# Optimization experiments

Hardware: AMD Instinct MI355X
Metric: run time of the kernel (lower is better)

## Reference

```python
import jax, jax.numpy as jnp
import numpy as np

RADIUS = 0.2
NSAMPLE = 32


def setup_inputs() -> dict:
    key = jax.random.key(0)
    k1, k2 = jax.random.split(key)
    B, N = 8, 4096
    xyz = jax.random.uniform(k1, (B, N, 3), dtype=jnp.float32)
    xyz_new = jax.random.uniform(k2, (B, N, 3), dtype=jnp.float32)  # ignored by forward, kept for signature fidelity
    return {"xyz": xyz, "xyz_new": xyz_new}


def _ball_query(radius, nsample, xyz, new_xyz):
    # xyz: [B, N, 3] source points; new_xyz: [B, M, 3] query centers.
    # Returns idx: [B, M, nsample] int32, matching pointnet2 CUDA ball_query:
    # first `nsample` indices j (in increasing j order) with ||q - p_j||^2 < r^2;
    # unused slots are filled with the first valid index.
    B, N, _ = xyz.shape
    sq_src = jnp.sum(xyz * xyz, axis=-1)          # [B, N]
    sq_q = jnp.sum(new_xyz * new_xyz, axis=-1)    # [B, M]
    # d2[b, m, n] = ||q_m - p_n||^2
    d2 = sq_q[:, :, None] + sq_src[:, None, :] - 2.0 * jnp.einsum(
        "bmc,bnc->bmn", new_xyz, xyz)             # [B, M, N]
    mask = d2 < (radius * radius)                 # [B, M, N] bool
    # key = index j when within radius, else sentinel N (sorts to the end)
    idx_range = jnp.arange(N, dtype=jnp.int32)
    keys = jnp.where(mask, idx_range[None, None, :], jnp.int32(N))
    sorted_keys = jnp.sort(keys, axis=-1)[..., :nsample]  # [B, M, nsample]
    first = sorted_keys[..., 0:1]                 # first valid index (pad value)
    idx = jnp.where(sorted_keys < N, sorted_keys, first)
    return idx.astype(jnp.int32)


def reference(xyz, xyz_new):
    # Faithful to the module: ball_query(radius, nsample, xyz, xyz) — xyz_new unused.
    return _ball_query(RADIUS, NSAMPLE, xyz, xyz)
```

## Files before the change

kernel.cpp:

```cpp
#include <hip/hip_runtime.h>
#include <cstdint>


#define BQ_N   4096
#define BQ_B   8
#define BQ_NS  32
#define BQ_R2  0.04f

__device__ __forceinline__ float sq_plain(float x, float y, float z) {
    float r, t;
    asm("v_mul_f32 %0, %2, %2\n\t"
        "v_mul_f32 %1, %3, %3\n\t"
        "v_add_f32 %0, %0, %1\n\t"
        "v_mul_f32 %1, %4, %4\n\t"
        "v_add_f32 %0, %0, %1"
        : "=&v"(r), "=&v"(t)
        : "v"(x), "v"(y), "v"(z));
    return r;
}

__device__ __forceinline__ float d2_mixed(float qx, float qy, float qz, float sqq,
                                          float sx, float sy, float sz, float sqs) {
    float r, t;
    asm("v_mul_f32 %0, %2, %5\n\t"
        "v_fma_f32 %0, %3, %6, %0\n\t"
        "v_fma_f32 %0, %4, %7, %0\n\t"
        "v_add_f32 %0, %0, %0\n\t"
        "v_add_f32 %1, %8, %9\n\t"
        "v_sub_f32 %0, %1, %0"
        : "=&v"(r), "=&v"(t)
        : "v"(qx), "v"(qy), "v"(qz), "v"(sx), "v"(sy), "v"(sz),
          "v"(sqq), "v"(sqs));
    return r;
}

__device__ __forceinline__ void scan_chunk1(const float4* pts, int lane,
                                            float4 q, int c,
                                            uint64_t& word, int& found) {
    #pragma unroll
    for (int u = 0; u < 4; ++u) {
        const int k = (c << 2) + u;
        const float4 s = pts[(k << 6) + lane];
        const float d2 = d2_mixed(q.x, q.y, q.z, q.w, s.x, s.y, s.z, s.w);
        const uint64_t bal = __ballot(d2 < BQ_R2);
        if (lane == k) word = bal;
        found += (int)__popcll(bal);
    }
}

__device__ __forceinline__ void emit_query(int* orow, int lane, uint64_t word) {
    const int cnt = __popcll(word);
    int incl = cnt;
    #pragma unroll
    for (int off = 1; off < 64; off <<= 1) {
        const int t = __shfl_up(incl, off);
        if (lane >= off) incl += t;
    }
    const int pre   = incl - cnt;
    const int total = __shfl(incl, 63);

    int first;
    const uint64_t nz = __ballot(word != 0ull);
    if (nz == 0ull) {
        first = BQ_N;
    } else {
        const int fl = __builtin_ctzll(nz);
        const uint64_t fw = __shfl(word, fl);
        first = (fl << 6) + __builtin_ctzll(fw);
    }

    uint64_t w = word;
    int pos = pre;
    while (w != 0ull && pos < BQ_NS) {
        const int bit = __builtin_ctzll(w);
        orow[pos] = (lane << 6) + bit;
        w &= (w - 1);
        ++pos;
    }
    if (lane == 0) {
        for (int p = total; p < BQ_NS; ++p) orow[p] = first;
    }
}

__global__ __launch_bounds__(256, 2)
void ball_query_kernel(const float* __restrict__ xyz, int* __restrict__ out)
{
    __shared__ float4 pts[BQ_N];

    const int b     = blockIdx.x >> 6;
    const int qbase = (blockIdx.x & 63) << 6;
    const float* __restrict__ src = xyz + (size_t)b * BQ_N * 3;

    for (int j = threadIdx.x; j < BQ_N; j += 256) {
        const float x = src[3 * j + 0];
        const float y = src[3 * j + 1];
        const float z = src[3 * j + 2];
        pts[j] = make_float4(x, y, z, sq_plain(x, y, z));
    }
    __syncthreads();

    const int lane = threadIdx.x & 63;
    const int wid  = threadIdx.x >> 6;
    int* __restrict__ outb = out + (size_t)(b * BQ_N) * BQ_NS;

    for (int p = 0; p < 8; ++p) {
        const int m0 = qbase + (wid << 4) + p;
        const int m1 = m0 + 8;
        const float4 q0 = pts[m0];
        const float4 q1 = pts[m1];

        uint64_t word0 = 0, word1 = 0;
        int found0 = 0, found1 = 0;

        int c = 0;
        while (c < 16) {
            #pragma unroll
            for (int u = 0; u < 4; ++u) {
                const int k = (c << 2) + u;
                const float4 s = pts[(k << 6) + lane];
                const float d20 = d2_mixed(q0.x, q0.y, q0.z, q0.w,
                                           s.x, s.y, s.z, s.w);
                const float d21 = d2_mixed(q1.x, q1.y, q1.z, q1.w,
                                           s.x, s.y, s.z, s.w);
                const uint64_t bal0 = __ballot(d20 < BQ_R2);
                const uint64_t bal1 = __ballot(d21 < BQ_R2);
                if (lane == k) { word0 = bal0; word1 = bal1; }
                found0 += (int)__popcll(bal0);
                found1 += (int)__popcll(bal1);
            }
            ++c;
            if (found0 >= BQ_NS || found1 >= BQ_NS) break;
        }
        for (int c0 = c; c0 < 16 && found0 < BQ_NS; ++c0)
            scan_chunk1(pts, lane, q0, c0, word0, found0);
        for (int c1 = c; c1 < 16 && found1 < BQ_NS; ++c1)
            scan_chunk1(pts, lane, q1, c1, word1, found1);

        emit_query(outb + (size_t)m0 * BQ_NS, lane, word0);
        emit_query(outb + (size_t)m1 * BQ_NS, lane, word1);
    }
}

extern "C" void kernel_launch(void* const* d_in, const int* in_sizes, int n_in,
                              void* d_out, int out_size, void* d_ws, size_t ws_size,
                              hipStream_t stream)
{
    const float* xyz = (const float*)d_in[0];
    int* out = (int*)d_out;
    hipLaunchKernelGGL(ball_query_kernel, dim3(BQ_B * 64), dim3(256), 0, stream,
                       xyz, out);
}
```

Baseline: 89.39 us.

## Halve shared point tile and double grid with two-phase scan per block

```diff
diff --git a/kernel.cpp b/kernel.cpp
--- a/kernel.cpp
+++ b/kernel.cpp
@@ -2,10 +2,11 @@
 #include <cstdint>
 
 
-#define BQ_N   4096
-#define BQ_B   8
-#define BQ_NS  32
-#define BQ_R2  0.04f
+#define BQ_N    4096
+#define BQ_HALF 2048
+#define BQ_B    8
+#define BQ_NS   32
+#define BQ_R2   0.04f
 
 __device__ __forceinline__ float sq_plain(float x, float y, float z) {
     float r, t;
@@ -34,18 +35,46 @@
     return r;
 }
 
-__device__ __forceinline__ void scan_chunk1(const float4* pts, int lane,
-                                            float4 q, int c,
-                                            uint64_t& word, int& found) {
+__device__ __forceinline__ void scan1(const float4* pts, int lane,
+                                      const float4& q, int c,
+                                      uint64_t& word, int& found) {
     #pragma unroll
     for (int u = 0; u < 4; ++u) {
         const int k = (c << 2) + u;
-        const float4 s = pts[(k << 6) + lane];
+        const float4 s = pts[((k & 31) << 6) + lane];
         const float d2 = d2_mixed(q.x, q.y, q.z, q.w, s.x, s.y, s.z, s.w);
         const uint64_t bal = __ballot(d2 < BQ_R2);
         if (lane == k) word = bal;
         found += (int)__popcll(bal);
     }
+}
+
+__device__ __forceinline__ void scan2(const float4* pts, int lane,
+                                      const float4& q0, const float4& q1,
+                                      int c0, int c1,
+                                      uint64_t& w0, uint64_t& w1,
+                                      int& f0, int& f1) {
+    int c = c0;
+    while (c < c1) {
+        #pragma unroll
+        for (int u = 0; u < 4; ++u) {
+            const int k = (c << 2) + u;
+            const float4 s = pts[((k & 31) << 6) + lane];
+            const float d20 = d2_mixed(q0.x, q0.y, q0.z, q0.w,
+                                       s.x, s.y, s.z, s.w);
+            const float d21 = d2_mixed(q1.x, q1.y, q1.z, q1.w,
+                                       s.x, s.y, s.z, s.w);
+            const uint64_t b0 = __ballot(d20 < BQ_R2);
+            const uint64_t b1 = __ballot(d21 < BQ_R2);
+            if (lane == k) { w0 = b0; w1 = b1; }
+            f0 += (int)__popcll(b0);
+            f1 += (int)__popcll(b1);
+        }
+        ++c;
+        if (f0 >= BQ_NS || f1 >= BQ_NS) break;
+    }
+    for (int ca = c; ca < c1 && f0 < BQ_NS; ++ca) scan1(pts, lane, q0, ca, w0, f0);
+    for (int cb = c; cb < c1 && f1 < BQ_NS; ++cb) scan1(pts, lane, q1, cb, w1, f1);
 }
 
 __device__ __forceinline__ void emit_query(int* orow, int lane, uint64_t word) {
@@ -77,21 +106,32 @@
         w &= (w - 1);
         ++pos;
     }
-    if (lane == 0) {
-        for (int p = total; p < BQ_NS; ++p) orow[p] = first;
-    }
+    if (lane >= total && lane < BQ_NS) orow[lane] = first;
 }
 
-__global__ __launch_bounds__(256, 2)
+__global__ __launch_bounds__(256, 4)
 void ball_query_kernel(const float* __restrict__ xyz, int* __restrict__ out)
 {
-    __shared__ float4 pts[BQ_N];
+    __shared__ float4 pts[BQ_HALF];
 
-    const int b     = blockIdx.x >> 6;
-    const int qbase = (blockIdx.x & 63) << 6;
+    const int b     = blockIdx.x >> 7;
+    const int qbase = (blockIdx.x & 127) << 5;
     const float* __restrict__ src = xyz + (size_t)b * BQ_N * 3;
+    const int lane = threadIdx.x & 63;
+    const int wid  = threadIdx.x >> 6;
+    int* __restrict__ outb = out + (size_t)(b * BQ_N) * BQ_NS;
 
-    for (int j = threadIdx.x; j < BQ_N; j += 256) {
+    float4 Q[8];
+    #pragma unroll
+    for (int j = 0; j < 8; ++j) {
+        const int m = qbase + (wid << 3) + j;
+        const float x = src[3 * m + 0];
+        const float y = src[3 * m + 1];
+        const float z = src[3 * m + 2];
+        Q[j] = make_float4(x, y, z, sq_plain(x, y, z));
+    }
+
+    for (int j = threadIdx.x; j < BQ_HALF; j += 256) {
         const float x = src[3 * j + 0];
         const float y = src[3 * j + 1];
         const float z = src[3 * j + 2];
@@ -99,45 +139,41 @@
     }
     __syncthreads();
 
-    const int lane = threadIdx.x & 63;
-    const int wid  = threadIdx.x >> 6;
-    int* __restrict__ outb = out + (size_t)(b * BQ_N) * BQ_NS;
+    uint64_t W[8] = {0, 0, 0, 0, 0, 0, 0, 0};
+    int      F[8] = {0, 0, 0, 0, 0, 0, 0, 0};
 
-    for (int p = 0; p < 8; ++p) {
-        const int m0 = qbase + (wid << 4) + p;
-        const int m1 = m0 + 8;
-        const float4 q0 = pts[m0];
-        const float4 q1 = pts[m1];
+    #pragma unroll
+    for (int p = 0; p < 4; ++p)
+        scan2(pts, lane, Q[p], Q[p + 4], 0, 8, W[p], W[p + 4], F[p], F[p + 4]);
 
-        uint64_t word0 = 0, word1 = 0;
-        int found0 = 0, found1 = 0;
+    __syncthreads();
+    for (int j = threadIdx.x; j < BQ_HALF; j += 256) {
+        const int g = BQ_HALF + j;
+        const float x = src[3 * g + 0];
+        const float y = src[3 * g + 1];
+        const float z = src[3 * g + 2];
+        pts[j] = make_float4(x, y, z, sq_plain(x, y, z));
+    }
+    __syncthreads();
 
-        int c = 0;
-        while (c < 16) {
-            #pragma unroll
-            for (int u = 0; u < 4; ++u) {
-                const int k = (c << 2) + u;
-                const float4 s = pts[(k << 6) + lane];
-                const float d20 = d2_mixed(q0.x, q0.y, q0.z, q0.w,
-                                           s.x, s.y, s.z, s.w);
-                const float d21 = d2_mixed(q1.x, q1.y, q1.z, q1.w,
-                                           s.x, s.y, s.z, s.w);
-                const uint64_t bal0 = __ballot(d20 < BQ_R2);
-                const uint64_t bal1 = __ballot(d21 < BQ_R2);
-                if (lane == k) { word0 = bal0; word1 = bal1; }
-                found0 += (int)__popcll(bal0);
-                found1 += (int)__popcll(bal1);
-            }
-            ++c;
-            if (found0 >= BQ_NS || found1 >= BQ_NS) break;
+    #pragma unroll
+    for (int p = 0; p < 4; ++p) {
+        if (F[p] < BQ_NS && F[p + 4] < BQ_NS) {
+            scan2(pts, lane, Q[p], Q[p + 4], 8, 16,
+                  W[p], W[p + 4], F[p], F[p + 4]);
+        } else if (F[p] < BQ_NS) {
+            for (int ca = 8; ca < 16 && F[p] < BQ_NS; ++ca)
+                scan1(pts, lane, Q[p], ca, W[p], F[p]);
+        } else if (F[p + 4] < BQ_NS) {
+            for (int cb = 8; cb < 16 && F[p + 4] < BQ_NS; ++cb)
+                scan1(pts, lane, Q[p + 4], cb, W[p + 4], F[p + 4]);
         }
-        for (int c0 = c; c0 < 16 && found0 < BQ_NS; ++c0)
-            scan_chunk1(pts, lane, q0, c0, word0, found0);
-        for (int c1 = c; c1 < 16 && found1 < BQ_NS; ++c1)
-            scan_chunk1(pts, lane, q1, c1, word1, found1);
+    }
 
-        emit_query(outb + (size_t)m0 * BQ_NS, lane, word0);
-        emit_query(outb + (size_t)m1 * BQ_NS, lane, word1);
+    #pragma unroll
+    for (int j = 0; j < 8; ++j) {
+        const int m = qbase + (wid << 3) + j;
+        emit_query(outb + (size_t)m * BQ_NS, lane, W[j]);
     }
 }
 
@@ -147,6 +183,6 @@
 {
     const float* xyz = (const float*)d_in[0];
     int* out = (int*)d_out;
-    hipLaunchKernelGGL(ball_query_kernel, dim3(BQ_B * 64), dim3(256), 0, stream,
+    hipLaunchKernelGGL(ball_query_kernel, dim3(1024), dim3(256), 0, stream,
                        xyz, out);
 }
```

Result: faster. 84.06 us (-6.0%).
